# Performance work log

Measured on AMD Instinct MI355X. Metric: run time of the kernel, lower is better.

Reference implementation:

```python
import jax, jax.numpy as jnp
import numpy as np

V, E, H = 50000, 300, 512
T, BIO, BIO_E = 9, 10, 64
REL_E, R = 128, 50
B, L = 16, 128


def _lstm(x, wih, whh, bih, bhh):
    # x: [B, L, E]; PyTorch gate order i, f, g, o
    h0 = jnp.zeros((x.shape[0], whh.shape[1]), x.dtype)
    def step(carry, xt):
        h, c = carry
        g = xt @ wih.T + h @ whh.T + (bih + bhh)
        i, f, gg, o = jnp.split(g, 4, axis=-1)
        c = jax.nn.sigmoid(f) * c + jax.nn.sigmoid(i) * jnp.tanh(gg)
        h = jax.nn.sigmoid(o) * jnp.tanh(c)
        return (h, c), h
    _, hs = jax.lax.scan(step, (h0, h0), jnp.swapaxes(x, 0, 1))
    return jnp.swapaxes(hs, 0, 1)


def _crf_nll(emi, tags, mask, trans, start, end):
    # torchcrf-style linear-chain CRF NLL, mean reduction. emi: [B,L,T]
    mf = mask.astype(emi.dtype)
    ar = jnp.arange(emi.shape[0])
    emi_t = jnp.swapaxes(emi, 0, 1)   # [L,B,T]
    tags_t = jnp.swapaxes(tags, 0, 1)
    mf_t = jnp.swapaxes(mf, 0, 1)
    num0 = start[tags_t[0]] + emi_t[0][ar, tags_t[0]]
    def num_step(carry, inp):
        prev, score = carry
        e_t, t_t, m_t = inp
        score = score + (trans[prev, t_t] + e_t[ar, t_t]) * m_t
        prev = jnp.where(m_t > 0, t_t, prev)
        return (prev, score), None
    (last, num), _ = jax.lax.scan(num_step, (tags_t[0], num0), (emi_t[1:], tags_t[1:], mf_t[1:]))
    num = num + end[last]
    def den_step(alpha, inp):
        e_t, m_t = inp
        nxt = jax.nn.logsumexp(alpha[:, :, None] + trans[None] + e_t[:, None, :], axis=1)
        return jnp.where(m_t[:, None] > 0, nxt, alpha), None
    alpha, _ = jax.lax.scan(den_step, start[None] + emi_t[0], (emi_t[1:], mf_t[1:]))
    den = jax.nn.logsumexp(alpha + end[None], axis=1)
    return -jnp.mean(num - den)


def setup_inputs() -> dict:
    key = jax.random.key(0)
    ks = jax.random.split(key, 24)
    lengths = jax.random.randint(ks[0], (B,), L // 2, L + 1)
    tok = jax.random.randint(ks[1], (B, L), 1, V)
    tokens = jnp.where(jnp.arange(L)[None, :] < lengths[:, None], tok, 0)  # 0 = <pad>
    n = lambda k, shp, s=0.05: jax.random.normal(k, shp, dtype=jnp.float32) * s
    z = lambda shp: jnp.zeros(shp, jnp.float32)
    return dict(
        tokens=tokens,
        bio_gold=jax.random.randint(ks[2], (B, L), 0, T),
        selection_gold=jax.random.randint(ks[3], (B, L, R, L), 0, 2).astype(jnp.int32),
        is_train=1,
        word_emb=n(ks[4], (V, E), 0.02),
        rel_emb=n(ks[5], (R, REL_E), 0.1),
        bio_emb=n(ks[6], (BIO, BIO_E), 0.1),
        w_ih_f=n(ks[7], (4 * H, E)), w_hh_f=n(ks[8], (4 * H, H)),
        b_ih_f=n(ks[9], (4 * H,)), b_hh_f=n(ks[10], (4 * H,)),
        w_ih_b=n(ks[11], (4 * H, E)), w_hh_b=n(ks[12], (4 * H, H)),
        b_ih_b=n(ks[13], (4 * H,)), b_hh_b=n(ks[14], (4 * H,)),
        emission_w=n(ks[15], (T, H)), emission_b=z((T,)),
        sel_u_w=n(ks[16], (REL_E, H + BIO_E)), sel_u_b=z((REL_E,)),
        sel_v_w=n(ks[17], (REL_E, H + BIO_E)), sel_v_b=z((REL_E,)),
        sel_uv_w=n(ks[18], (REL_E, 2 * REL_E)), sel_uv_b=z((REL_E,)),
        crf_trans=n(ks[19], (T, T), 0.1),
        crf_start=n(ks[20], (T,), 0.1),
        crf_end=n(ks[21], (T,), 0.1),
    )


def reference(tokens, bio_gold, selection_gold, is_train, word_emb, rel_emb, bio_emb,
              w_ih_f, w_hh_f, b_ih_f, b_hh_f, w_ih_b, w_hh_b, b_ih_b, b_hh_b,
              emission_w, emission_b, sel_u_w, sel_u_b, sel_v_w, sel_v_b,
              sel_uv_w, sel_uv_b, crf_trans, crf_start, crf_end):
    mask = tokens != 0
    emb = word_emb[tokens]                                 # [B,L,E]
    hf = _lstm(emb, w_ih_f, w_hh_f, b_ih_f, b_hh_f)
    hb = _lstm(emb[:, ::-1], w_ih_b, w_hh_b, b_ih_b, b_hh_b)[:, ::-1]
    o = (hf + hb) * 0.5                                    # avg of the two directions
    emi = o @ emission_w.T + emission_b                    # [B,L,T]
    crf_loss = _crf_nll(emi, bio_gold, mask, crf_trans, crf_start, crf_end)
    oc = jnp.concatenate([o, bio_emb[bio_gold]], axis=-1)  # [B,L,H+BIO_E]
    u = jax.nn.relu(oc @ sel_u_w.T + sel_u_b)              # [B,L,REL_E]
    v = jax.nn.relu(oc @ sel_v_w.T + sel_v_b)
    # linear(concat(u_j, v_i)) == u_j @ W1.T + v_i @ W2.T  (fused, avoids [B,L,L,2R])
    w1, w2 = sel_uv_w[:, :REL_E], sel_uv_w[:, REL_E:]
    uv = jax.nn.relu((u @ w1.T)[:, None, :, :] + (v @ w2.T)[:, :, None, :] + sel_uv_b)  # [B,L,L,REL_E]
    logits = jnp.einsum('bijh,rh->birj', uv, rel_emb)      # [B,L,R,L]
    g = selection_gold.astype(logits.dtype)
    bce = jnp.maximum(logits, 0) - logits * g + jnp.log1p(jnp.exp(-jnp.abs(logits)))
    pm = (mask[:, :, None] & mask[:, None, :])[:, :, None, :].astype(logits.dtype)
    sel_loss = jnp.sum(bce * pm) / jnp.sum(mask).astype(logits.dtype)
    return crf_loss + sel_loss
```

## Files before the change

kernel.cpp:

```cpp
#include <hip/hip_runtime.h>
#include <math.h>

#define NB   16
#define SL   128
#define ED   300
#define HD   512
#define G4   2048
#define NT   9
#define BE   64
#define RE   128
#define NR   50
#define OCD  576
#define NTOK 2048

__device__ __forceinline__ float sigf(float x){ return 1.0f/(1.0f + __expf(-x)); }

__global__ __launch_bounds__(256) void gather_emb_k(const int* __restrict__ tokens,
                                                    const float* __restrict__ word_emb,
                                                    float* __restrict__ emb)
{
    int idx = blockIdx.x*256 + threadIdx.x;
    if (idx < NTOK*ED){
        int row = idx / ED;
        int k = idx - row*ED;
        emb[idx] = word_emb[tokens[row]*ED + k];
    }
}

template<int TM>
__device__ __forceinline__ void gemm_body(const float* __restrict__ A, int lda,
                                          const float* __restrict__ Bm, int ldb,
                                          float* __restrict__ C, int ldc,
                                          int N, int K,
                                          const float* __restrict__ bias1,
                                          const float* __restrict__ bias2,
                                          int do_relu, int m_blk, int n_blk)
{
    constexpr int TR = TM/16;
    __shared__ float As[16][TM+4];
    __shared__ float Bs[16][68];
    const int t = threadIdx.x;
    const int tm = (t >> 4) * TR;
    const int tn = (t & 15) * 4;
    float acc[TR][4];
    #pragma unroll
    for (int i=0;i<TR;++i){ acc[i][0]=0.f; acc[i][1]=0.f; acc[i][2]=0.f; acc[i][3]=0.f; }

    const int kc = (K + 15) >> 4;
    for (int ck = 0; ck < kc; ++ck){
        const int k0 = ck << 4;
        __syncthreads();
        #pragma unroll
        for (int it = 0; it < TM/64; ++it){
            int task = t + it*256;
            int m = task >> 2, q = task & 3;
            int kk = k0 + q*4;
            float4 v = make_float4(0.f,0.f,0.f,0.f);
            const float* ap = A + (size_t)(m_blk + m)*lda + kk;
            if (kk + 3 < K) v = *(const float4*)ap;
            else {
                if (kk   < K) v.x = ap[0];
                if (kk+1 < K) v.y = ap[1];
                if (kk+2 < K) v.z = ap[2];
            }
            As[q*4+0][m] = v.x; As[q*4+1][m] = v.y; As[q*4+2][m] = v.z; As[q*4+3][m] = v.w;
        }
        {
            int n = t >> 2, q = t & 3;
            int kk = k0 + q*4;
            int gn = n_blk + n;
            float4 v = make_float4(0.f,0.f,0.f,0.f);
            if (gn < N){
                const float* bp = Bm + (size_t)gn*ldb + kk;
                if (kk + 3 < K) v = *(const float4*)bp;
                else {
                    if (kk   < K) v.x = bp[0];
                    if (kk+1 < K) v.y = bp[1];
                    if (kk+2 < K) v.z = bp[2];
                }
            }
            Bs[q*4+0][n] = v.x; Bs[q*4+1][n] = v.y; Bs[q*4+2][n] = v.z; Bs[q*4+3][n] = v.w;
        }
        __syncthreads();
        #pragma unroll
        for (int k = 0; k < 16; ++k){
            float4 b4 = *(const float4*)&Bs[k][tn];
            float bn[4] = {b4.x, b4.y, b4.z, b4.w};
            #pragma unroll
            for (int i = 0; i < TR/4; ++i){
                float4 a4 = *(const float4*)&As[k][tm + i*4];
                float am[4] = {a4.x, a4.y, a4.z, a4.w};
                #pragma unroll
                for (int mm = 0; mm < 4; ++mm){
                    #pragma unroll
                    for (int nn = 0; nn < 4; ++nn)
                        acc[i*4+mm][nn] += am[mm]*bn[nn];
                }
            }
        }
    }
    float bv[4];
    #pragma unroll
    for (int nn=0;nn<4;++nn){
        int gn = n_blk + tn + nn;
        float bb = 0.f;
        if (gn < N){
            if (bias1) bb += bias1[gn];
            if (bias2) bb += bias2[gn];
        }
        bv[nn] = bb;
    }
    bool vec = ((ldc & 3) == 0) && (n_blk + tn + 3 < N);
    #pragma unroll
    for (int mm = 0; mm < TR; ++mm){
        int gm = m_blk + tm + mm;
        float r0 = acc[mm][0] + bv[0];
        float r1 = acc[mm][1] + bv[1];
        float r2 = acc[mm][2] + bv[2];
        float r3 = acc[mm][3] + bv[3];
        if (do_relu){ r0=fmaxf(r0,0.f); r1=fmaxf(r1,0.f); r2=fmaxf(r2,0.f); r3=fmaxf(r3,0.f); }
        if (vec){
            *(float4*)(C + (size_t)gm*ldc + n_blk + tn) = make_float4(r0,r1,r2,r3);
        } else {
            int gn = n_blk + tn;
            if (gn   < N) C[(size_t)gm*ldc + gn  ] = r0;
            if (gn+1 < N) C[(size_t)gm*ldc + gn+1] = r1;
            if (gn+2 < N) C[(size_t)gm*ldc + gn+2] = r2;
            if (gn+3 < N) C[(size_t)gm*ldc + gn+3] = r3;
        }
    }
}

template<int TM>
__global__ __launch_bounds__(256) void gemm_k(const float* __restrict__ A, int lda,
                                              const float* __restrict__ Bm, int ldb,
                                              float* __restrict__ C, int ldc,
                                              int N, int K,
                                              const float* __restrict__ bias1,
                                              const float* __restrict__ bias2,
                                              int do_relu)
{
    gemm_body<TM>(A, lda, Bm, ldb, C, ldc, N, K, bias1, bias2, do_relu,
                  blockIdx.x * TM, blockIdx.y * 64);
}

template<int TM>
__global__ __launch_bounds__(256) void gemm_dual_k(const float* __restrict__ A0, const float* __restrict__ A1, int lda,
                                                   const float* __restrict__ B0, const float* __restrict__ B1, int ldb,
                                                   float* __restrict__ C0, float* __restrict__ C1, int ldc,
                                                   int N, int K,
                                                   const float* __restrict__ bias0, const float* __restrict__ bias1,
                                                   int do_relu)
{
    const int z = blockIdx.z;
    gemm_body<TM>(z ? A1 : A0, lda, z ? B1 : B0, ldb, z ? C1 : C0, ldc, N, K,
                  z ? bias1 : bias0, nullptr, do_relu, blockIdx.x * TM, blockIdx.y * 64);
}

__global__ __launch_bounds__(256, 1) void lstm_k(const float* __restrict__ xwf,
                                                 const float* __restrict__ xwb,
                                                 const float* __restrict__ whhf,
                                                 const float* __restrict__ whhb,
                                                 unsigned long long* __restrict__ hteam,
                                                 float* __restrict__ hf_all,
                                                 float* __restrict__ hb_all)
{
    __shared__ __align__(16) float h_s[4*HD];
    __shared__ __align__(16) float part[8*256];
    __shared__ float gates_s[256];
    __shared__ float cst[64];
    const int wg   = blockIdx.x;
    const int team = wg >> 5;
    const int rank = wg & 31;
    const int d    = team & 1;
    const int b0   = (team >> 1) * 4;
    const int t    = threadIdx.x;
    const int wv   = t >> 6;
    const int lane = t & 63;
    const int rg   = t & 31;
    const int kc   = t >> 5;
    const int lr0  = rg*2, lr1 = rg*2 + 1;
    const int grow0 = (lr0 >> 4)*HD + rank*16 + (lr0 & 15);
    const int grow1 = (lr1 >> 4)*HD + rank*16 + (lr1 & 15);
    const float* whh = d ? whhb : whhf;
    const float* xw  = d ? xwb  : xwf;
    float* hall      = d ? hb_all : hf_all;
    unsigned long long* hT = hteam + (size_t)team*2*(4*HD);

    float4 w0[16], w1[16];
    {
        const float* wp0 = whh + (size_t)grow0*HD + kc*64;
        const float* wp1 = whh + (size_t)grow1*HD + kc*64;
        #pragma unroll
        for (int q = 0; q < 16; ++q){ w0[q] = *(const float4*)(wp0 + q*4);
                                      w1[q] = *(const float4*)(wp1 + q*4); }
    }
    const int rrow = t >> 2, rb = t & 3;
    const int growr = (rrow >> 4)*HD + rank*16 + (rrow & 15);
    const int ahl = t & 15, ab = t >> 4;
    const int hidx_a = rank*16 + ahl;
    const int sb = wv*128 + lane;

    if (t < 64) cst[t] = 0.f;
    __syncthreads();

    int par = 0;
    for (int s = 0; s < SL; ++s){
        const int tx = d ? (SL-1 - s) : s;
        const float xval = xw[(size_t)((b0 + rb)*SL + tx)*G4 + growr];
        {
            const unsigned long long* src = hT + (size_t)par*(4*HD);
            unsigned long long v[8];
            const unsigned want = (unsigned)s;
            for (;;){
                #pragma unroll
                for (int i = 0; i < 8; ++i)
                    v[i] = __hip_atomic_load(&src[(i>>1)*512 + (i&1)*64 + sb],
                                             __ATOMIC_RELAXED, __HIP_MEMORY_SCOPE_AGENT);
                bool ok = true;
                #pragma unroll
                for (int i = 0; i < 8; ++i) ok = ok && ((unsigned)(v[i] >> 32) == want);
                if (ok) break;
                __builtin_amdgcn_s_sleep(1);
            }
            #pragma unroll
            for (int i = 0; i < 8; ++i)
                h_s[(i>>1)*HD + (i&1)*64 + sb] = __uint_as_float((unsigned)v[i]);
        }
        {
            float a0[4] = {0.f,0.f,0.f,0.f};
            float a1[4] = {0.f,0.f,0.f,0.f};
            #pragma unroll
            for (int q = 0; q < 16; ++q){
                float4 wa = w0[q], wb = w1[q];
                #pragma unroll
                for (int b = 0; b < 4; ++b){
                    float4 h4 = *(const float4*)(h_s + b*HD + kc*64 + q*4);
                    a0[b] += wa.x*h4.x + wa.y*h4.y + wa.z*h4.z + wa.w*h4.w;
                    a1[b] += wb.x*h4.x + wb.y*h4.y + wb.z*h4.z + wb.w*h4.w;
                }
            }
            *(float4*)&part[kc*256 + lr0*4] = make_float4(a0[0],a0[1],a0[2],a0[3]);
            *(float4*)&part[kc*256 + lr1*4] = make_float4(a1[0],a1[1],a1[2],a1[3]);
        }
        __syncthreads();
        {
            float gsum = 0.f;
            #pragma unroll
            for (int c = 0; c < 8; ++c) gsum += part[c*256 + t];
            gates_s[t] = gsum + xval;
        }
        __syncthreads();
        if (t < 64){
            float gi = gates_s[((0*16) + ahl)*4 + ab];
            float gf = gates_s[((1*16) + ahl)*4 + ab];
            float gc = gates_s[((2*16) + ahl)*4 + ab];
            float gov = gates_s[((3*16) + ahl)*4 + ab];
            float cp = cst[t];
            float cn = sigf(gf)*cp + sigf(gi)*tanhf(gc);
            float hn = sigf(gov)*tanhf(cn);
            cst[t] = cn;
            unsigned long long pk = ((unsigned long long)(unsigned)(s+1) << 32)
                                  | (unsigned long long)__float_as_uint(hn);
            __hip_atomic_store(&hT[(size_t)(par^1)*(4*HD) + ab*HD + hidx_a], pk,
                               __ATOMIC_RELAXED, __HIP_MEMORY_SCOPE_AGENT);
            hall[(size_t)((b0 + ab)*SL + tx)*HD + hidx_a] = hn;
        }
        par ^= 1;
    }
}

__global__ __launch_bounds__(256) void combine_k(const float* __restrict__ hf,
                                                 const float* __restrict__ hb,
                                                 const int* __restrict__ bio_gold,
                                                 const float* __restrict__ bio_emb,
                                                 float* __restrict__ oc)
{
    int idx = blockIdx.x*256 + threadIdx.x;
    if (idx >= NTOK*144) return;
    int row = idx / 144;
    int c4 = (idx - row*144) * 4;
    float4 v;
    if (c4 < HD){
        float4 a = *(const float4*)(hf + (size_t)row*HD + c4);
        float4 b = *(const float4*)(hb + (size_t)row*HD + c4);
        v = make_float4(0.5f*(a.x+b.x), 0.5f*(a.y+b.y), 0.5f*(a.z+b.z), 0.5f*(a.w+b.w));
    } else {
        int bg = bio_gold[row];
        v = *(const float4*)(bio_emb + bg*BE + (c4 - HD));
    }
    *(float4*)(oc + (size_t)row*OCD + c4) = v;
}

__global__ __launch_bounds__(64) void crf_k(const float* __restrict__ emi,
                                            const int* __restrict__ tags,
                                            const int* __restrict__ tokens,
                                            const float* __restrict__ trans,
                                            const float* __restrict__ startv,
                                            const float* __restrict__ endv,
                                            float* __restrict__ out_crf)
{
    __shared__ float al[16];
    const int b = blockIdx.x, lane = threadIdx.x;
    unsigned long long m0 = __ballot(tokens[b*SL + lane] != 0);
    unsigned long long m1 = __ballot(tokens[b*SL + 64 + lane] != 0);
    const int len = __popcll(m0) + __popcll(m1);
    float npart = 0.f;
    #pragma unroll
    for (int half = 0; half < 2; ++half){
        int tt = lane + half*64;
        if (tt >= 1 && tt < len){
            int tp = tags[b*SL + tt - 1], tc = tags[b*SL + tt];
            npart += trans[tp*NT + tc] + emi[(size_t)(b*SL + tt)*NT + tc];
        }
    }
    #pragma unroll
    for (int off = 32; off > 0; off >>= 1) npart += __shfl_down(npart, off);
    float tr[NT]; float alpha = -1e30f;
    if (lane < NT){
        #pragma unroll
        for (int i = 0; i < NT; ++i) tr[i] = trans[i*NT + lane];
        alpha = startv[lane] + emi[(size_t)(b*SL)*NT + lane];
    }
    for (int tt = 1; tt < SL; ++tt){
        if (lane < NT) al[lane] = alpha;
        __syncthreads();
        if (lane < NT && tt < len){
            float mx = -1e30f;
            #pragma unroll
            for (int i = 0; i < NT; ++i) mx = fmaxf(mx, al[i] + tr[i]);
            float se = 0.f;
            #pragma unroll
            for (int i = 0; i < NT; ++i) se += __expf(al[i] + tr[i] - mx);
            alpha = mx + __logf(se) + emi[(size_t)(b*SL + tt)*NT + lane];
        }
        __syncthreads();
    }
    if (lane < NT) al[lane] = alpha + endv[lane];
    __syncthreads();
    if (lane == 0){
        float mx = -1e30f;
        for (int i = 0; i < NT; ++i) mx = fmaxf(mx, al[i]);
        float se = 0.f;
        for (int i = 0; i < NT; ++i) se += __expf(al[i] - mx);
        float den = mx + __logf(se);
        int t0g = tags[b*SL];
        float num = startv[t0g] + emi[(size_t)(b*SL)*NT + t0g] + npart;
        num += endv[tags[b*SL + len - 1]];
        atomicAdd(out_crf, -(num - den) * (1.0f/16.0f));
    }
}

__global__ __launch_bounds__(256) void msum_k(const int* __restrict__ tokens, float* __restrict__ out_m)
{
    __shared__ int rr[4];
    int t = threadIdx.x;
    int cnt = 0;
    for (int i = t; i < NTOK; i += 256) cnt += (tokens[i] != 0) ? 1 : 0;
    #pragma unroll
    for (int off = 32; off > 0; off >>= 1) cnt += __shfl_down(cnt, off);
    if ((t & 63) == 0) rr[t >> 6] = cnt;
    __syncthreads();
    if (t == 0) out_m[0] = (float)(rr[0]+rr[1]+rr[2]+rr[3]);
}

__global__ __launch_bounds__(256) void sel_k(const float* __restrict__ U2,
                                             const float* __restrict__ V2,
                                             const float* __restrict__ uvb,
                                             const float* __restrict__ rel_emb,
                                             const int* __restrict__ gold,
                                             const int* __restrict__ tokens,
                                             float* __restrict__ out_sel)
{
    __shared__ float ret_s[RE][52];
    __shared__ float pt_s[RE][68];
    __shared__ float vb_s[RE];
    __shared__ float mk_s[64];
    __shared__ float red_s[4];
    const int jt = blockIdx.x, qi = blockIdx.y, b = blockIdx.z;
    const int t = threadIdx.x;
    if (tokens[b*SL + qi] == 0) return;
    if (t < 32){
        float4 v4 = *(const float4*)(V2 + (size_t)(b*SL + qi)*RE + t*4);
        float4 b4 = *(const float4*)(uvb + t*4);
        vb_s[t*4+0] = v4.x + b4.x; vb_s[t*4+1] = v4.y + b4.y;
        vb_s[t*4+2] = v4.z + b4.z; vb_s[t*4+3] = v4.w + b4.w;
    }
    if (t < 64) mk_s[t] = (tokens[b*SL + jt*64 + t] != 0) ? 1.f : 0.f;
    {
        int r = t & 63;
        for (int q = t >> 6; q < 32; q += 4){
            if (r < NR){
                float4 e4 = *(const float4*)(rel_emb + (size_t)r*RE + q*4);
                ret_s[q*4+0][r] = e4.x; ret_s[q*4+1][r] = e4.y;
                ret_s[q*4+2][r] = e4.z; ret_s[q*4+3][r] = e4.w;
            } else if (r < 64){
                ret_s[q*4+0][r] = 0.f; ret_s[q*4+1][r] = 0.f;
                ret_s[q*4+2][r] = 0.f; ret_s[q*4+3][r] = 0.f;
            }
        }
    }
    __syncthreads();
    {
        int j = t & 63;
        for (int q = t >> 6; q < 32; q += 4){
            float4 u4 = *(const float4*)(U2 + (size_t)(b*SL + jt*64 + j)*RE + q*4);
            pt_s[q*4+0][j] = fmaxf(u4.x + vb_s[q*4+0], 0.f);
            pt_s[q*4+1][j] = fmaxf(u4.y + vb_s[q*4+1], 0.f);
            pt_s[q*4+2][j] = fmaxf(u4.z + vb_s[q*4+2], 0.f);
            pt_s[q*4+3][j] = fmaxf(u4.w + vb_s[q*4+3], 0.f);
        }
    }
    __syncthreads();
    const int mj = (t & 15) * 4;
    const int nr = (t >> 4) * 4;
    float accv[4][4];
    #pragma unroll
    for (int i=0;i<4;++i){ accv[i][0]=0.f; accv[i][1]=0.f; accv[i][2]=0.f; accv[i][3]=0.f; }
    #pragma unroll 4
    for (int k = 0; k < RE; ++k){
        float4 aj = *(const float4*)&pt_s[k][mj];
        float4 br = *(const float4*)&ret_s[k][nr];
        float am[4] = {aj.x, aj.y, aj.z, aj.w};
        float bn[4] = {br.x, br.y, br.z, br.w};
        #pragma unroll
        for (int mm = 0; mm < 4; ++mm){
            #pragma unroll
            for (int nn = 0; nn < 4; ++nn)
                accv[mm][nn] += am[mm]*bn[nn];
        }
    }
    float lsum = 0.f;
    #pragma unroll
    for (int nn = 0; nn < 4; ++nn){
        int r = nr + nn;
        if (r < NR){
            const int* gp = gold + (size_t)((b*SL + qi)*NR + r)*SL + jt*64 + mj;
            #pragma unroll
            for (int mm = 0; mm < 4; ++mm){
                float l = accv[mm][nn];
                float g = (float)gp[mm];
                float bce = fmaxf(l, 0.f) - l*g + __logf(1.f + __expf(-fabsf(l)));
                lsum += bce * mk_s[mj + mm];
            }
        }
    }
    #pragma unroll
    for (int off = 32; off > 0; off >>= 1) lsum += __shfl_down(lsum, off);
    if ((t & 63) == 0) red_s[t >> 6] = lsum;
    __syncthreads();
    if (t == 0) atomicAdd(out_sel, red_s[0]+red_s[1]+red_s[2]+red_s[3]);
}

__global__ void finalize_k(const float* __restrict__ accum, float* __restrict__ out)
{
    if (threadIdx.x == 0 && blockIdx.x == 0) out[0] = accum[0] + accum[1] / accum[2];
}

extern "C" void kernel_launch(void* const* d_in, const int* in_sizes, int n_in,
                              void* d_out, int out_size, void* d_ws, size_t ws_size,
                              hipStream_t stream)
{
    const int*   tokens    = (const int*)  d_in[0];
    const int*   bio_gold  = (const int*)  d_in[1];
    const int*   sel_gold  = (const int*)  d_in[2];
    const float* word_emb  = (const float*)d_in[4];
    const float* rel_emb   = (const float*)d_in[5];
    const float* bio_emb   = (const float*)d_in[6];
    const float* w_ih_f    = (const float*)d_in[7];
    const float* w_hh_f    = (const float*)d_in[8];
    const float* b_ih_f    = (const float*)d_in[9];
    const float* b_hh_f    = (const float*)d_in[10];
    const float* w_ih_b    = (const float*)d_in[11];
    const float* w_hh_b    = (const float*)d_in[12];
    const float* b_ih_b    = (const float*)d_in[13];
    const float* b_hh_b    = (const float*)d_in[14];
    const float* emission_w= (const float*)d_in[15];
    const float* emission_b= (const float*)d_in[16];
    const float* sel_u_w   = (const float*)d_in[17];
    const float* sel_u_b   = (const float*)d_in[18];
    const float* sel_v_w   = (const float*)d_in[19];
    const float* sel_v_b   = (const float*)d_in[20];
    const float* sel_uv_w  = (const float*)d_in[21];
    const float* sel_uv_b  = (const float*)d_in[22];
    const float* crf_trans = (const float*)d_in[23];
    const float* crf_start = (const float*)d_in[24];
    const float* crf_end   = (const float*)d_in[25];
    (void)in_sizes; (void)n_in; (void)out_size; (void)ws_size;

    float* ws     = (float*)d_ws;
    float* emb    = ws;
    float* xwf    = emb    + (size_t)NTOK*ED;
    float* xwb    = xwf    + (size_t)NTOK*G4;
    float* hf_all = xwb    + (size_t)NTOK*G4;
    float* hb_all = hf_all + (size_t)NTOK*HD;
    float* oc     = hb_all + (size_t)NTOK*HD;
    float* emi    = oc     + (size_t)NTOK*OCD;
    float* u_     = emi    + (size_t)NTOK*NT;
    float* v_     = u_     + (size_t)NTOK*RE;
    float* U2     = v_     + (size_t)NTOK*RE;
    float* V2     = U2     + (size_t)NTOK*RE;
    float* accum  = V2     + (size_t)NTOK*RE;

    unsigned long long* hteam = (unsigned long long*)emb;

    hipMemsetAsync(accum, 0, 4*sizeof(float), stream);

    gather_emb_k<<<(NTOK*ED + 255)/256, 256, 0, stream>>>(tokens, word_emb, emb);

    dim3 gw(NTOK/128, G4/64);
    gemm_k<128><<<gw, 256, 0, stream>>>(emb, ED, w_ih_f, ED, xwf, G4, G4, ED, b_ih_f, b_hh_f, 0);
    gemm_k<128><<<gw, 256, 0, stream>>>(emb, ED, w_ih_b, ED, xwb, G4, G4, ED, b_ih_b, b_hh_b, 0);

    hipMemsetAsync(hteam, 0, (size_t)8*2*(4*HD)*sizeof(unsigned long long), stream);

    {
        const float *p_xwf = xwf, *p_xwb = xwb, *p_whf = w_hh_f, *p_whb = w_hh_b;
        unsigned long long* p_ht = hteam;
        float *p_hf = hf_all, *p_hb = hb_all;
        void* args[7] = {&p_xwf, &p_xwb, &p_whf, &p_whb, &p_ht, &p_hf, &p_hb};
        hipLaunchCooperativeKernel(lstm_k, dim3(256), dim3(256), args, 0u, stream);
    }

    combine_k<<<(NTOK*144 + 255)/256, 256, 0, stream>>>(hf_all, hb_all, bio_gold, bio_emb, oc);

    gemm_k<64><<<dim3(NTOK/64, 1), 256, 0, stream>>>(oc, OCD, emission_w, HD, emi, NT, NT, HD, emission_b, nullptr, 0);
    gemm_dual_k<64><<<dim3(NTOK/64, 2, 2), 256, 0, stream>>>(oc, oc, OCD, sel_u_w, sel_v_w, OCD,
                                                             u_, v_, RE, RE, OCD, sel_u_b, sel_v_b, 1);
    gemm_dual_k<64><<<dim3(NTOK/64, 2, 2), 256, 0, stream>>>(u_, v_, RE, sel_uv_w, sel_uv_w + RE, 2*RE,
                                                             U2, V2, RE, RE, RE, nullptr, nullptr, 0);

    crf_k<<<NB, 64, 0, stream>>>(emi, bio_gold, tokens, crf_trans, crf_start, crf_end, accum + 0);
    msum_k<<<1, 256, 0, stream>>>(tokens, accum + 2);
    sel_k<<<dim3(2, SL, NB), 256, 0, stream>>>(U2, V2, sel_uv_b, rel_emb, sel_gold, tokens, accum + 1);

    finalize_k<<<1, 1, 0, stream>>>(accum, (float*)d_out);
}
```

Baseline: 1.045 ms.

## Interleave LSTM directions per team, fuse embedding gather into input GEMM

Each cooperative LSTM workgroup now handles both forward and backward directions for 2 batch rows instead of one direction for 4 rows. It prefetches the backward hidden state while the forward step computes, so one direction's cross-team exchange latency is hidden behind the other's math. The embedding gather is fused into a single input-projection GEMM launch covering both directions, and the mask count is folded into the CRF kernel, which now uses warp shuffles instead of shared memory and barriers. The trade-offs are doubled recurrent weights held in registers, which raises register pressure, and two sequential half-sized steps per timestep with extra barriers.

```diff
diff --git a/kernel.cpp b/kernel.cpp
--- a/kernel.cpp
+++ b/kernel.cpp
@@ -14,18 +14,6 @@
 #define NTOK 2048
 
 __device__ __forceinline__ float sigf(float x){ return 1.0f/(1.0f + __expf(-x)); }
-
-__global__ __launch_bounds__(256) void gather_emb_k(const int* __restrict__ tokens,
-                                                    const float* __restrict__ word_emb,
-                                                    float* __restrict__ emb)
-{
-    int idx = blockIdx.x*256 + threadIdx.x;
-    if (idx < NTOK*ED){
-        int row = idx / ED;
-        int k = idx - row*ED;
-        emb[idx] = word_emb[tokens[row]*ED + k];
-    }
-}
 
 template<int TM>
 __device__ __forceinline__ void gemm_body(const float* __restrict__ A, int lda,
@@ -157,6 +145,90 @@
                   z ? bias1 : bias0, nullptr, do_relu, blockIdx.x * TM, blockIdx.y * 64);
 }
 
+__global__ __launch_bounds__(256) void gemm_emb_k(const int* __restrict__ tokens,
+                                                  const float* __restrict__ word_emb,
+                                                  const float* __restrict__ B0, const float* __restrict__ B1,
+                                                  float* __restrict__ C0, float* __restrict__ C1,
+                                                  const float* __restrict__ bi0a, const float* __restrict__ bi0b,
+                                                  const float* __restrict__ bi1a, const float* __restrict__ bi1b)
+{
+    __shared__ float As[16][132];
+    __shared__ float Bs[16][68];
+    const int z = blockIdx.z;
+    const float* Bm = z ? B1 : B0;
+    float* C       = z ? C1 : C0;
+    const float* ba = z ? bi1a : bi0a;
+    const float* bb = z ? bi1b : bi0b;
+    const int t = threadIdx.x;
+    const int m_blk = blockIdx.x * 128;
+    const int n_blk = blockIdx.y * 64;
+    const int tm = (t >> 4) * 8;
+    const int tn = (t & 15) * 4;
+    float acc[8][4];
+    #pragma unroll
+    for (int i=0;i<8;++i){ acc[i][0]=0.f; acc[i][1]=0.f; acc[i][2]=0.f; acc[i][3]=0.f; }
+
+    for (int ck = 0; ck < 19; ++ck){
+        const int k0 = ck << 4;
+        __syncthreads();
+        #pragma unroll
+        for (int it = 0; it < 2; ++it){
+            int task = t + it*256;
+            int m = task >> 2, q = task & 3;
+            int kk = k0 + q*4;
+            const int tok = tokens[m_blk + m];
+            const float* ap = word_emb + (size_t)tok*ED + kk;
+            float4 v = make_float4(0.f,0.f,0.f,0.f);
+            if (kk + 3 < ED) v = *(const float4*)ap;
+            else {
+                if (kk   < ED) v.x = ap[0];
+                if (kk+1 < ED) v.y = ap[1];
+                if (kk+2 < ED) v.z = ap[2];
+            }
+            As[q*4+0][m] = v.x; As[q*4+1][m] = v.y; As[q*4+2][m] = v.z; As[q*4+3][m] = v.w;
+        }
+        {
+            int n = t >> 2, q = t & 3;
+            int kk = k0 + q*4;
+            const float* bp = Bm + (size_t)(n_blk + n)*ED + kk;
+            float4 v = make_float4(0.f,0.f,0.f,0.f);
+            if (kk + 3 < ED) v = *(const float4*)bp;
+            else {
+                if (kk   < ED) v.x = bp[0];
+                if (kk+1 < ED) v.y = bp[1];
+                if (kk+2 < ED) v.z = bp[2];
+            }
+            Bs[q*4+0][n] = v.x; Bs[q*4+1][n] = v.y; Bs[q*4+2][n] = v.z; Bs[q*4+3][n] = v.w;
+        }
+        __syncthreads();
+        #pragma unroll
+        for (int k = 0; k < 16; ++k){
+            float4 b4 = *(const float4*)&Bs[k][tn];
+            float bn[4] = {b4.x, b4.y, b4.z, b4.w};
+            #pragma unroll
+            for (int i = 0; i < 2; ++i){
+                float4 a4 = *(const float4*)&As[k][tm + i*4];
+                float am[4] = {a4.x, a4.y, a4.z, a4.w};
+                #pragma unroll
+                for (int mm = 0; mm < 4; ++mm){
+                    #pragma unroll
+                    for (int nn = 0; nn < 4; ++nn)
+                        acc[i*4+mm][nn] += am[mm]*bn[nn];
+                }
+            }
+        }
+    }
+    float bv[4];
+    #pragma unroll
+    for (int nn=0;nn<4;++nn){ int gn = n_blk + tn + nn; bv[nn] = ba[gn] + bb[gn]; }
+    #pragma unroll
+    for (int mm = 0; mm < 8; ++mm){
+        int gm = m_blk + tm + mm;
+        *(float4*)(C + (size_t)gm*G4 + n_blk + tn) =
+            make_float4(acc[mm][0]+bv[0], acc[mm][1]+bv[1], acc[mm][2]+bv[2], acc[mm][3]+bv[3]);
+    }
+}
+
 __global__ __launch_bounds__(256, 1) void lstm_k(const float* __restrict__ xwf,
                                                  const float* __restrict__ xwb,
                                                  const float* __restrict__ whhf,
@@ -165,15 +237,15 @@
                                                  float* __restrict__ hf_all,
                                                  float* __restrict__ hb_all)
 {
-    __shared__ __align__(16) float h_s[4*HD];
-    __shared__ __align__(16) float part[8*256];
-    __shared__ float gates_s[256];
+    __shared__ __align__(16) float h_sf[2*HD];
+    __shared__ __align__(16) float h_sb[2*HD];
+    __shared__ __align__(16) float part[8*128];
+    __shared__ float gates_s[128];
     __shared__ float cst[64];
     const int wg   = blockIdx.x;
     const int team = wg >> 5;
     const int rank = wg & 31;
-    const int d    = team & 1;
-    const int b0   = (team >> 1) * 4;
+    const int b0   = team * 2;
     const int t    = threadIdx.x;
     const int wv   = t >> 6;
     const int lane = t & 63;
@@ -182,89 +254,154 @@
     const int lr0  = rg*2, lr1 = rg*2 + 1;
     const int grow0 = (lr0 >> 4)*HD + rank*16 + (lr0 & 15);
     const int grow1 = (lr1 >> 4)*HD + rank*16 + (lr1 & 15);
-    const float* whh = d ? whhb : whhf;
-    const float* xw  = d ? xwb  : xwf;
-    float* hall      = d ? hb_all : hf_all;
-    unsigned long long* hT = hteam + (size_t)team*2*(4*HD);
-
-    float4 w0[16], w1[16];
+    unsigned long long* hTf = hteam + (size_t)(team*2 + 0)*2*1024;
+    unsigned long long* hTb = hteam + (size_t)(team*2 + 1)*2*1024;
+
+    float4 wf0[16], wf1[16], wb0[16], wb1[16];
     {
-        const float* wp0 = whh + (size_t)grow0*HD + kc*64;
-        const float* wp1 = whh + (size_t)grow1*HD + kc*64;
-        #pragma unroll
-        for (int q = 0; q < 16; ++q){ w0[q] = *(const float4*)(wp0 + q*4);
-                                      w1[q] = *(const float4*)(wp1 + q*4); }
-    }
-    const int rrow = t >> 2, rb = t & 3;
+        const float* p0 = whhf + (size_t)grow0*HD + kc*64;
+        const float* p1 = whhf + (size_t)grow1*HD + kc*64;
+        const float* p2 = whhb + (size_t)grow0*HD + kc*64;
+        const float* p3 = whhb + (size_t)grow1*HD + kc*64;
+        #pragma unroll
+        for (int q = 0; q < 16; ++q){
+            wf0[q] = *(const float4*)(p0 + q*4);
+            wf1[q] = *(const float4*)(p1 + q*4);
+            wb0[q] = *(const float4*)(p2 + q*4);
+            wb1[q] = *(const float4*)(p3 + q*4);
+        }
+    }
+    const int rrow = t >> 1, rb2 = t & 1;
     const int growr = (rrow >> 4)*HD + rank*16 + (rrow & 15);
-    const int ahl = t & 15, ab = t >> 4;
+    const int ahl = t >> 1, ab2 = t & 1;
     const int hidx_a = rank*16 + ahl;
-    const int sb = wv*128 + lane;
+    const int s0 = wv*128 + lane;
 
     if (t < 64) cst[t] = 0.f;
     __syncthreads();
 
     int par = 0;
     for (int s = 0; s < SL; ++s){
-        const int tx = d ? (SL-1 - s) : s;
-        const float xval = xw[(size_t)((b0 + rb)*SL + tx)*G4 + growr];
+        float xval_f = 0.f, xval_b = 0.f;
+        if (t < 128){
+            xval_f = xwf[(size_t)((b0 + rb2)*SL + s)*G4 + growr];
+            xval_b = xwb[(size_t)((b0 + rb2)*SL + (SL-1 - s))*G4 + growr];
+        }
         {
-            const unsigned long long* src = hT + (size_t)par*(4*HD);
-            unsigned long long v[8];
+            const unsigned long long* src = hTf + (size_t)par*1024;
+            unsigned long long v0,v1,v2,v3;
             const unsigned want = (unsigned)s;
             for (;;){
-                #pragma unroll
-                for (int i = 0; i < 8; ++i)
-                    v[i] = __hip_atomic_load(&src[(i>>1)*512 + (i&1)*64 + sb],
-                                             __ATOMIC_RELAXED, __HIP_MEMORY_SCOPE_AGENT);
-                bool ok = true;
-                #pragma unroll
-                for (int i = 0; i < 8; ++i) ok = ok && ((unsigned)(v[i] >> 32) == want);
-                if (ok) break;
+                v0 = __hip_atomic_load(&src[      s0     ], __ATOMIC_RELAXED, __HIP_MEMORY_SCOPE_AGENT);
+                v1 = __hip_atomic_load(&src[      s0 + 64], __ATOMIC_RELAXED, __HIP_MEMORY_SCOPE_AGENT);
+                v2 = __hip_atomic_load(&src[512 + s0     ], __ATOMIC_RELAXED, __HIP_MEMORY_SCOPE_AGENT);
+                v3 = __hip_atomic_load(&src[512 + s0 + 64], __ATOMIC_RELAXED, __HIP_MEMORY_SCOPE_AGENT);
+                if (((unsigned)(v0>>32)==want) & ((unsigned)(v1>>32)==want) &
+                    ((unsigned)(v2>>32)==want) & ((unsigned)(v3>>32)==want)) break;
                 __builtin_amdgcn_s_sleep(1);
             }
-            #pragma unroll
-            for (int i = 0; i < 8; ++i)
-                h_s[(i>>1)*HD + (i&1)*64 + sb] = __uint_as_float((unsigned)v[i]);
-        }
+            h_sf[     s0     ] = __uint_as_float((unsigned)v0);
+            h_sf[     s0 + 64] = __uint_as_float((unsigned)v1);
+            h_sf[HD + s0     ] = __uint_as_float((unsigned)v2);
+            h_sf[HD + s0 + 64] = __uint_as_float((unsigned)v3);
+        }
+        const unsigned long long* srcb = hTb + (size_t)par*1024;
+        unsigned long long p0 = __hip_atomic_load(&srcb[      s0     ], __ATOMIC_RELAXED, __HIP_MEMORY_SCOPE_AGENT);
+        unsigned long long p1 = __hip_atomic_load(&srcb[      s0 + 64], __ATOMIC_RELAXED, __HIP_MEMORY_SCOPE_AGENT);
+        unsigned long long p2 = __hip_atomic_load(&srcb[512 + s0     ], __ATOMIC_RELAXED, __HIP_MEMORY_SCOPE_AGENT);
+        unsigned long long p3 = __hip_atomic_load(&srcb[512 + s0 + 64], __ATOMIC_RELAXED, __HIP_MEMORY_SCOPE_AGENT);
         {
-            float a0[4] = {0.f,0.f,0.f,0.f};
-            float a1[4] = {0.f,0.f,0.f,0.f};
+            float a00=0.f,a01=0.f,a10=0.f,a11=0.f;
             #pragma unroll
             for (int q = 0; q < 16; ++q){
-                float4 wa = w0[q], wb = w1[q];
-                #pragma unroll
-                for (int b = 0; b < 4; ++b){
-                    float4 h4 = *(const float4*)(h_s + b*HD + kc*64 + q*4);
-                    a0[b] += wa.x*h4.x + wa.y*h4.y + wa.z*h4.z + wa.w*h4.w;
-                    a1[b] += wb.x*h4.x + wb.y*h4.y + wb.z*h4.z + wb.w*h4.w;
-                }
-            }
-            *(float4*)&part[kc*256 + lr0*4] = make_float4(a0[0],a0[1],a0[2],a0[3]);
-            *(float4*)&part[kc*256 + lr1*4] = make_float4(a1[0],a1[1],a1[2],a1[3]);
-        }
-        __syncthreads();
-        {
-            float gsum = 0.f;
-            #pragma unroll
-            for (int c = 0; c < 8; ++c) gsum += part[c*256 + t];
-            gates_s[t] = gsum + xval;
-        }
-        __syncthreads();
-        if (t < 64){
-            float gi = gates_s[((0*16) + ahl)*4 + ab];
-            float gf = gates_s[((1*16) + ahl)*4 + ab];
-            float gc = gates_s[((2*16) + ahl)*4 + ab];
-            float gov = gates_s[((3*16) + ahl)*4 + ab];
+                float4 wa = wf0[q], wb = wf1[q];
+                float4 h0 = *(const float4*)(h_sf + 0*HD + kc*64 + q*4);
+                float4 h1 = *(const float4*)(h_sf + 1*HD + kc*64 + q*4);
+                a00 += wa.x*h0.x + wa.y*h0.y + wa.z*h0.z + wa.w*h0.w;
+                a01 += wa.x*h1.x + wa.y*h1.y + wa.z*h1.z + wa.w*h1.w;
+                a10 += wb.x*h0.x + wb.y*h0.y + wb.z*h0.z + wb.w*h0.w;
+                a11 += wb.x*h1.x + wb.y*h1.y + wb.z*h1.z + wb.w*h1.w;
+            }
+            *(float4*)&part[kc*128 + lr0*2] = make_float4(a00,a01,a10,a11);
+        }
+        __syncthreads();
+        if (t < 128){
+            float g = 0.f;
+            #pragma unroll
+            for (int c = 0; c < 8; ++c) g += part[c*128 + t];
+            gates_s[t] = g + xval_f;
+        }
+        __syncthreads();
+        if (t < 32){
+            float gi = gates_s[(0*16 + ahl)*2 + ab2];
+            float gf = gates_s[(1*16 + ahl)*2 + ab2];
+            float gc = gates_s[(2*16 + ahl)*2 + ab2];
+            float go_ = gates_s[(3*16 + ahl)*2 + ab2];
             float cp = cst[t];
             float cn = sigf(gf)*cp + sigf(gi)*tanhf(gc);
-            float hn = sigf(gov)*tanhf(cn);
+            float hn = sigf(go_)*tanhf(cn);
             cst[t] = cn;
             unsigned long long pk = ((unsigned long long)(unsigned)(s+1) << 32)
                                   | (unsigned long long)__float_as_uint(hn);
-            __hip_atomic_store(&hT[(size_t)(par^1)*(4*HD) + ab*HD + hidx_a], pk,
+            __hip_atomic_store(&hTf[(size_t)(par^1)*1024 + ab2*512 + hidx_a], pk,
                                __ATOMIC_RELAXED, __HIP_MEMORY_SCOPE_AGENT);
-            hall[(size_t)((b0 + ab)*SL + tx)*HD + hidx_a] = hn;
+            hf_all[(size_t)((b0 + ab2)*SL + s)*HD + hidx_a] = hn;
+        }
+        {
+            const unsigned want = (unsigned)s;
+            if (!(((unsigned)(p0>>32)==want) & ((unsigned)(p1>>32)==want) &
+                  ((unsigned)(p2>>32)==want) & ((unsigned)(p3>>32)==want))){
+                for (;;){
+                    p0 = __hip_atomic_load(&srcb[      s0     ], __ATOMIC_RELAXED, __HIP_MEMORY_SCOPE_AGENT);
+                    p1 = __hip_atomic_load(&srcb[      s0 + 64], __ATOMIC_RELAXED, __HIP_MEMORY_SCOPE_AGENT);
+                    p2 = __hip_atomic_load(&srcb[512 + s0     ], __ATOMIC_RELAXED, __HIP_MEMORY_SCOPE_AGENT);
+                    p3 = __hip_atomic_load(&srcb[512 + s0 + 64], __ATOMIC_RELAXED, __HIP_MEMORY_SCOPE_AGENT);
+                    if (((unsigned)(p0>>32)==want) & ((unsigned)(p1>>32)==want) &
+                        ((unsigned)(p2>>32)==want) & ((unsigned)(p3>>32)==want)) break;
+                    __builtin_amdgcn_s_sleep(1);
+                }
+            }
+            h_sb[     s0     ] = __uint_as_float((unsigned)p0);
+            h_sb[     s0 + 64] = __uint_as_float((unsigned)p1);
+            h_sb[HD + s0     ] = __uint_as_float((unsigned)p2);
+            h_sb[HD + s0 + 64] = __uint_as_float((unsigned)p3);
+        }
+        {
+            float a00=0.f,a01=0.f,a10=0.f,a11=0.f;
+            #pragma unroll
+            for (int q = 0; q < 16; ++q){
+                float4 wa = wb0[q], wb = wb1[q];
+                float4 h0 = *(const float4*)(h_sb + 0*HD + kc*64 + q*4);
+                float4 h1 = *(const float4*)(h_sb + 1*HD + kc*64 + q*4);
+                a00 += wa.x*h0.x + wa.y*h0.y + wa.z*h0.z + wa.w*h0.w;
+                a01 += wa.x*h1.x + wa.y*h1.y + wa.z*h1.z + wa.w*h1.w;
+                a10 += wb.x*h0.x + wb.y*h0.y + wb.z*h0.z + wb.w*h0.w;
+                a11 += wb.x*h1.x + wb.y*h1.y + wb.z*h1.z + wb.w*h1.w;
+            }
+            *(float4*)&part[kc*128 + lr0*2] = make_float4(a00,a01,a10,a11);
+        }
+        __syncthreads();
+        if (t < 128){
+            float g = 0.f;
+            #pragma unroll
+            for (int c = 0; c < 8; ++c) g += part[c*128 + t];
+            gates_s[t] = g + xval_b;
+        }
+        __syncthreads();
+        if (t < 32){
+            float gi = gates_s[(0*16 + ahl)*2 + ab2];
+            float gf = gates_s[(1*16 + ahl)*2 + ab2];
+            float gc = gates_s[(2*16 + ahl)*2 + ab2];
+            float go_ = gates_s[(3*16 + ahl)*2 + ab2];
+            float cp = cst[32 + t];
+            float cn = sigf(gf)*cp + sigf(gi)*tanhf(gc);
+            float hn = sigf(go_)*tanhf(cn);
+            cst[32 + t] = cn;
+            unsigned long long pk = ((unsigned long long)(unsigned)(s+1) << 32)
+                                  | (unsigned long long)__float_as_uint(hn);
+            __hip_atomic_store(&hTb[(size_t)(par^1)*1024 + ab2*512 + hidx_a], pk,
+                               __ATOMIC_RELAXED, __HIP_MEMORY_SCOPE_AGENT);
+            hb_all[(size_t)((b0 + ab2)*SL + (SL-1 - s))*HD + hidx_a] = hn;
         }
         par ^= 1;
     }
@@ -298,9 +435,9 @@
                                             const float* __restrict__ trans,
                                             const float* __restrict__ startv,
                                             const float* __restrict__ endv,
-                                            float* __restrict__ out_crf)
-{
-    __shared__ float al[16];
+                                            float* __restrict__ out_crf,
+                                            float* __restrict__ out_m)
+{
     const int b = blockIdx.x, lane = threadIdx.x;
     unsigned long long m0 = __ballot(tokens[b*SL + lane] != 0);
     unsigned long long m1 = __ballot(tokens[b*SL + 64 + lane] != 0);
@@ -323,8 +460,9 @@
         alpha = startv[lane] + emi[(size_t)(b*SL)*NT + lane];
     }
     for (int tt = 1; tt < SL; ++tt){
-        if (lane < NT) al[lane] = alpha;
-        __syncthreads();
+        float al[NT];
+        #pragma unroll
+        for (int i = 0; i < NT; ++i) al[i] = __shfl(alpha, i);
         if (lane < NT && tt < len){
             float mx = -1e30f;
             #pragma unroll
@@ -334,34 +472,25 @@
             for (int i = 0; i < NT; ++i) se += __expf(al[i] + tr[i] - mx);
             alpha = mx + __logf(se) + emi[(size_t)(b*SL + tt)*NT + lane];
         }
-        __syncthreads();
-    }
-    if (lane < NT) al[lane] = alpha + endv[lane];
-    __syncthreads();
+    }
+    float alf = (lane < NT) ? (alpha + endv[lane]) : -1e30f;
+    float alE[NT];
+    #pragma unroll
+    for (int i = 0; i < NT; ++i) alE[i] = __shfl(alf, i);
     if (lane == 0){
         float mx = -1e30f;
-        for (int i = 0; i < NT; ++i) mx = fmaxf(mx, al[i]);
+        #pragma unroll
+        for (int i = 0; i < NT; ++i) mx = fmaxf(mx, alE[i]);
         float se = 0.f;
-        for (int i = 0; i < NT; ++i) se += __expf(al[i] - mx);
+        #pragma unroll
+        for (int i = 0; i < NT; ++i) se += __expf(alE[i] - mx);
         float den = mx + __logf(se);
         int t0g = tags[b*SL];
         float num = startv[t0g] + emi[(size_t)(b*SL)*NT + t0g] + npart;
         num += endv[tags[b*SL + len - 1]];
         atomicAdd(out_crf, -(num - den) * (1.0f/16.0f));
-    }
-}
-
-__global__ __launch_bounds__(256) void msum_k(const int* __restrict__ tokens, float* __restrict__ out_m)
-{
-    __shared__ int rr[4];
-    int t = threadIdx.x;
-    int cnt = 0;
-    for (int i = t; i < NTOK; i += 256) cnt += (tokens[i] != 0) ? 1 : 0;
-    #pragma unroll
-    for (int off = 32; off > 0; off >>= 1) cnt += __shfl_down(cnt, off);
-    if ((t & 63) == 0) rr[t >> 6] = cnt;
-    __syncthreads();
-    if (t == 0) out_m[0] = (float)(rr[0]+rr[1]+rr[2]+rr[3]);
+        atomicAdd(out_m, (float)len);
+    }
 }
 
 __global__ __launch_bounds__(256) void sel_k(const float* __restrict__ U2,
@@ -505,14 +634,11 @@
     unsigned long long* hteam = (unsigned long long*)emb;
 
     hipMemsetAsync(accum, 0, 4*sizeof(float), stream);
-
-    gather_emb_k<<<(NTOK*ED + 255)/256, 256, 0, stream>>>(tokens, word_emb, emb);
-
-    dim3 gw(NTOK/128, G4/64);
-    gemm_k<128><<<gw, 256, 0, stream>>>(emb, ED, w_ih_f, ED, xwf, G4, G4, ED, b_ih_f, b_hh_f, 0);
-    gemm_k<128><<<gw, 256, 0, stream>>>(emb, ED, w_ih_b, ED, xwb, G4, G4, ED, b_ih_b, b_hh_b, 0);
-
-    hipMemsetAsync(hteam, 0, (size_t)8*2*(4*HD)*sizeof(unsigned long long), stream);
+    hipMemsetAsync(hteam, 0, (size_t)8*2*2*1024*sizeof(unsigned long long), stream);
+
+    gemm_emb_k<<<dim3(NTOK/128, G4/64, 2), 256, 0, stream>>>(tokens, word_emb,
+                                                             w_ih_f, w_ih_b, xwf, xwb,
+                                                             b_ih_f, b_hh_f, b_ih_b, b_hh_b);
 
     {
         const float *p_xwf = xwf, *p_xwb = xwb, *p_whf = w_hh_f, *p_whb = w_hh_b;
@@ -530,8 +656,7 @@
     gemm_dual_k<64><<<dim3(NTOK/64, 2, 2), 256, 0, stream>>>(u_, v_, RE, sel_uv_w, sel_uv_w + RE, 2*RE,
                                                              U2, V2, RE, RE, RE, nullptr, nullptr, 0);
 
-    crf_k<<<NB, 64, 0, stream>>>(emi, bio_gold, tokens, crf_trans, crf_start, crf_end, accum + 0);
-    msum_k<<<1, 256, 0, stream>>>(tokens, accum + 2);
+    crf_k<<<NB, 64, 0, stream>>>(emi, bio_gold, tokens, crf_trans, crf_start, crf_end, accum + 0, accum + 2);
     sel_k<<<dim3(2, SL, NB), 256, 0, stream>>>(U2, V2, sel_uv_b, rel_emb, sel_gold, tokens, accum + 1);
 
     finalize_k<<<1, 1, 0, stream>>>(accum, (float*)d_out);
```

After: 0.9996 ms. 4.4% less time.
